# Kernel tuning notes

Measured on AMD Instinct MI355X. Metric: run time of the kernel, lower is better.

The kernel has to match this reference:

```python
import jax, jax.numpy as jnp
from jax import lax
import numpy as np

N = 8000                      # number of input points (also padded unique-voxel count)
PC_RANGE = (-50.0, -50.0, -3.0, 50.0, 50.0, 3.0)
VOXEL = (0.25, 0.25, 6.0)     # cluster_voxel_size
CONN_DIST = 0.6               # connected_dist
GX = int(np.floor((PC_RANGE[3] - PC_RANGE[0]) / VOXEL[0])) + 1
GY = int(np.floor((PC_RANGE[4] - PC_RANGE[1]) / VOXEL[1])) + 1
GZ = int(np.floor((PC_RANGE[5] - PC_RANGE[2]) / VOXEL[2])) + 1


def setup_inputs() -> dict:
    key = jax.random.key(0)
    u = jax.random.uniform(key, (N, 3), dtype=jnp.float32)
    lo = jnp.array(PC_RANGE[:3], jnp.float32)
    hi = jnp.array(PC_RANGE[3:], jnp.float32)
    points = lo + u * (hi - lo)          # points spread over the full pc_range
    batch_idx = jnp.zeros((N,), jnp.int32)  # single batch (eval path)
    return {"points": points, "batch_idx": batch_idx}


def _voxel_ids(points, batch_idx):
    lo = jnp.array(PC_RANGE[:3], dtype=points.dtype)
    vs = jnp.array(VOXEL, dtype=points.dtype)
    coors = jnp.floor((points - lo) / vs).astype(jnp.int32)
    coors = jnp.clip(coors, 0, jnp.array([GX - 1, GY - 1, GZ - 1], jnp.int32))
    # linearize (batch, cx, cy, cz) -> single int id (equivalent to unique over rows)
    return ((batch_idx * GX + coors[:, 0]) * GY + coors[:, 1]) * GZ + coors[:, 2]


def reference(points, batch_idx):
    # ---- scatter_v2(mode='avg'): voxelize + per-voxel mean ----
    vid = _voxel_ids(points, batch_idx)
    _, inv = jnp.unique(vid, size=N, fill_value=-1, return_inverse=True)
    inv = inv.reshape(-1)
    ones = jnp.ones((N,), points.dtype)
    counts = jax.ops.segment_sum(ones, inv, num_segments=N)           # [N]
    centers = jax.ops.segment_sum(points, inv, num_segments=N) / jnp.maximum(counts, 1.0)[:, None]
    valid = counts > 0                                                # real (non-padded) voxels

    # ---- radius adjacency over xy of voxel centers ----
    xy = centers[:, :2]
    sq = jnp.sum(xy * xy, axis=1)
    d2 = sq[:, None] + sq[None, :] - 2.0 * (xy @ xy.T)
    dmat = jnp.sqrt(jnp.maximum(d2, 0.0))                             # [N,N]
    pair_valid = valid[:, None] & valid[None, :]
    adj = (jnp.where(pair_valid, dmat, jnp.inf) < CONN_DIST) | jnp.eye(N, dtype=bool)

    # ---- connected components via min-label propagation + pointer jumping ----
    labels0 = jnp.arange(N, dtype=jnp.int32)

    def body_fn(state):
        l, _ = state
        nl = jnp.min(jnp.where(adj, l[None, :], N), axis=1).astype(jnp.int32)
        nl = jnp.minimum(nl, nl[nl])  # pointer jump accelerates convergence
        return (nl, jnp.all(nl == l))

    labels, _ = lax.while_loop(lambda st: jnp.logical_not(st[1]), body_fn, (labels0, jnp.array(False)))

    # compress component roots to dense 0..K-1 in first-occurrence order
    # (scipy.connected_components labels components by min node index order);
    # padded slots are pushed after all real components.
    comp_key = jnp.where(valid, labels, labels + N)
    _, comp = jnp.unique(comp_key, size=N, fill_value=2 * N, return_inverse=True)
    comp = comp.reshape(-1).astype(jnp.int32)

    cluster_inds = comp[inv]                                          # per-point component id
    cls = jnp.zeros((N,), jnp.int32)                                  # modify_cluster_by_class, class 0
    cluster_inds_per_point = jnp.stack([cls, batch_idx, cluster_inds], axis=1)  # [N,3]
    valid_mask = jnp.ones((N,), bool)                                 # min_points=1 -> all kept
    return cluster_inds_per_point, valid_mask
```

## Files before the change

kernel.cpp:

```cpp
#include <hip/hip_runtime.h>
#include <math.h>
#include <limits.h>

#define NPTS   8000
#define GXD    401
#define GYD    401
#define GZD    2
#define MVOX   321602
#define TS     256
#define NTB    32

__global__ void k_vid(const float* __restrict__ pts, const int* __restrict__ batch,
                      int* __restrict__ vid, int* __restrict__ V) {
  int p = blockIdx.x * blockDim.x + threadIdx.x;
  if (p >= NPTS) return;
  float x = pts[3 * p + 0], y = pts[3 * p + 1], z = pts[3 * p + 2];
  int cx = (int)floorf((x - (-50.0f)) / 0.25f);
  int cy = (int)floorf((y - (-50.0f)) / 0.25f);
  int cz = (int)floorf((z - (-3.0f)) / 6.0f);
  cx = min(max(cx, 0), GXD - 1);
  cy = min(max(cy, 0), GYD - 1);
  cz = min(max(cz, 0), GZD - 1);
  int b = batch[p];
  int v = ((b * GXD + cx) * GYD + cy) * GZD + cz;
  v = min(max(v, 0), MVOX - 1);
  vid[p] = v;
  atomicMin(&V[v], p);
}

__global__ void k_rank(const int* __restrict__ vid, const int* __restrict__ V,
                       int* __restrict__ inv) {
  __shared__ int rs[TS];
  int t = threadIdx.x;
  int j = blockIdx.y * TS + t;
  int r = INT_MAX;
  if (j < NPTS) {
    int v = vid[j];
    r = (V[v] == j) ? v : INT_MAX;
  }
  rs[t] = r;
  __syncthreads();
  int p = blockIdx.x * blockDim.x + t;
  if (p >= NPTS) return;
  int v = vid[p];
  int c = 0;
  const int4* rs4 = (const int4*)rs;
  #pragma unroll 16
  for (int k4 = 0; k4 < TS / 4; ++k4) {
    int4 q = rs4[k4];
    c += (q.x < v) ? 1 : 0;
    c += (q.y < v) ? 1 : 0;
    c += (q.z < v) ? 1 : 0;
    c += (q.w < v) ? 1 : 0;
  }
  if (c) atomicAdd(&inv[p], c);
}

__global__ void k_accum(const float* __restrict__ pts, const int* __restrict__ inv,
                        float* __restrict__ cnt, float* __restrict__ sx,
                        float* __restrict__ sy, int* __restrict__ parent) {
  int p = blockIdx.x * blockDim.x + threadIdx.x;
  if (p >= NPTS) return;
  parent[p] = p;
  int s = inv[p];
  atomicAdd(&cnt[s], 1.0f);
  atomicAdd(&sx[s], pts[3 * p + 0]);
  atomicAdd(&sy[s], pts[3 * p + 1]);
}

__global__ void k_centers(const float* __restrict__ cnt, const float* __restrict__ sx,
                          const float* __restrict__ sy, float4* __restrict__ pk) {
  int u = blockIdx.x * blockDim.x + threadIdx.x;
  if (u >= NPTS) return;
  float c = cnt[u];
  float d = fmaxf(c, 1.0f);
  float X = sx[u] / d;
  float Y = sy[u] / d;
  if (c > 0.0f) pk[u] = make_float4(X, Y, X * X + Y * Y, 0.0f);
  else          pk[u] = make_float4(0.0f, 0.0f, 1e30f, 0.0f);
}

__device__ __forceinline__ int load_par(int* parent, int x) {
  return __hip_atomic_load(&parent[x], __ATOMIC_RELAXED, __HIP_MEMORY_SCOPE_AGENT);
}

__device__ void hook(int* parent, int u, int v) {
  int ru = u, rv = v;
  while (true) {
    int p;
    while ((p = load_par(parent, ru)) != ru) ru = p;
    while ((p = load_par(parent, rv)) != rv) rv = p;
    if (ru == rv) return;
    int hi = ru > rv ? ru : rv;
    int lo = ru ^ rv ^ hi;
    int old = atomicCAS(&parent[hi], hi, lo);
    if (old == hi) return;
    ru = lo; rv = old;
  }
}

__global__ void k_edges(const float4* __restrict__ pk, int* __restrict__ parent) {
  if (blockIdx.y < blockIdx.x) return;
  __shared__ float4 tile[TS];
  int t = threadIdx.x;
  int j0 = blockIdx.y * TS;
  int j = j0 + t;
  tile[t] = (j < NPTS) ? pk[j] : make_float4(0.0f, 0.0f, 1e30f, 0.0f);
  __syncthreads();
  int i = blockIdx.x * blockDim.x + t;
  if (i >= NPTS) return;
  float4 qi = pk[i];
  float xi = qi.x, yi = qi.y, si = qi.z;
  for (int kb = 0; kb < TS; kb += 64) {
    unsigned long long m = 0;
    #pragma unroll
    for (int k2 = 0; k2 < 64; ++k2) {
      float4 q = tile[kb + k2];
      float d2 = si + q.z - 2.0f * (xi * q.x + yi * q.y);
      if (d2 < 0.36f) m |= (1ull << k2);
    }
    while (m) {
      int k2 = __ffsll(m) - 1;
      m &= m - 1;
      hook(parent, i, j0 + kb + k2);
    }
  }
}

__global__ void k_flatten(const int* __restrict__ parent, int* __restrict__ labels) {
  int u = blockIdx.x * blockDim.x + threadIdx.x;
  if (u >= NPTS) return;
  int x = u, p;
  while ((p = parent[x]) != x) x = p;
  labels[u] = x;
}

__global__ void k_scan(const int* __restrict__ labels, const float* __restrict__ cnt,
                       int* __restrict__ compRank) {
  __shared__ int sc[1024];
  int t = threadIdx.x;
  int f[8];
  int s = 0;
  #pragma unroll
  for (int k = 0; k < 8; ++k) {
    int i = t * 8 + k;
    int fl = 0;
    if (i < NPTS) fl = (cnt[i] > 0.0f && labels[i] == i) ? 1 : 0;
    f[k] = fl; s += fl;
  }
  sc[t] = s;
  __syncthreads();
  for (int off = 1; off < 1024; off <<= 1) {
    int v = sc[t];
    int a = (t >= off) ? sc[t - off] : 0;
    __syncthreads();
    sc[t] = v + a;
    __syncthreads();
  }
  int excl = sc[t] - s;
  #pragma unroll
  for (int k = 0; k < 8; ++k) {
    int i = t * 8 + k;
    if (i < NPTS) { compRank[i] = excl; excl += f[k]; }
  }
}

__global__ void k_out(const int* __restrict__ inv, const int* __restrict__ labels,
                      const int* __restrict__ compRank, const int* __restrict__ batch,
                      int* __restrict__ out) {
  int p = blockIdx.x * blockDim.x + threadIdx.x;
  if (p >= NPTS) return;
  int lab = labels[inv[p]];
  int c = compRank[lab];
  out[3 * p + 0] = 0;
  out[3 * p + 1] = batch[p];
  out[3 * p + 2] = c;
  out[3 * NPTS + p] = 1;
}

extern "C" void kernel_launch(void* const* d_in, const int* in_sizes, int n_in,
                              void* d_out, int out_size, void* d_ws, size_t ws_size,
                              hipStream_t stream) {
  const float* pts   = (const float*)d_in[0];
  const int*   batch = (const int*)d_in[1];
  int* out = (int*)d_out;

  char* base = (char*)d_ws;
  size_t o = 0;
  int*    V       = (int*)(base + o);    o += ((size_t)MVOX * 4 + 255) & ~(size_t)255;
  int*    vid     = (int*)(base + o);    o += NPTS * 4;
  int*    inv     = (int*)(base + o);    o += NPTS * 4;
  float*  cnt     = (float*)(base + o);  o += NPTS * 4;
  float*  sx      = (float*)(base + o);  o += NPTS * 4;
  float*  sy      = (float*)(base + o);  o += NPTS * 4;
  float4* pk      = (float4*)(base + o); o += (size_t)NPTS * 16;
  int*    parent  = (int*)(base + o);    o += NPTS * 4;
  int*    labels  = (int*)(base + o);    o += NPTS * 4;
  int*    compRank= (int*)(base + o);    o += NPTS * 4;

  hipMemsetAsync(V, 0x7F, (size_t)MVOX * 4, stream);
  hipMemsetAsync(inv, 0, (size_t)4 * NPTS * 4, stream);

  dim3 b256(256);
  dim3 g1((NPTS + 255) / 256);
  dim3 g2(NTB, NTB);

  k_vid<<<g1, b256, 0, stream>>>(pts, batch, vid, V);
  k_rank<<<g2, b256, 0, stream>>>(vid, V, inv);
  k_accum<<<g1, b256, 0, stream>>>(pts, inv, cnt, sx, sy, parent);
  k_centers<<<g1, b256, 0, stream>>>(cnt, sx, sy, pk);
  k_edges<<<g2, b256, 0, stream>>>(pk, parent);
  k_flatten<<<g1, b256, 0, stream>>>(parent, labels);
  k_scan<<<1, 1024, 0, stream>>>(labels, cnt, compRank);
  k_out<<<g1, b256, 0, stream>>>(inv, labels, compRank, batch, out);
}
```

Before: 112.7 us.

## Fuse all voxelize and clustering stages into one cooperative persistent kernel

Replaces the two memsets and eight separate kernel launches with a single cooperative kernel of 256 blocks that runs each stage in turn, separated by grid-wide syncs. Workspace initialization moves into the kernel, and the rank and edge tile loops become grid-stride loops over block pairs. Flatten and scan run concurrently in one phase: block 0 scans root flags while the other blocks flatten labels. This removes per-launch overhead and memset calls, in exchange for grid.sync costs and a fixed occupancy requirement for a cooperative launch.

```diff
diff --git a/kernel.cpp b/kernel.cpp
--- a/kernel.cpp
+++ b/kernel.cpp
@@ -1,6 +1,9 @@
 #include <hip/hip_runtime.h>
+#include <hip/hip_cooperative_groups.h>
 #include <math.h>
 #include <limits.h>
+
+namespace cg = cooperative_groups;
 
 #define NPTS   8000
 #define GXD    401
@@ -9,76 +12,10 @@
 #define MVOX   321602
 #define TS     256
 #define NTB    32
-
-__global__ void k_vid(const float* __restrict__ pts, const int* __restrict__ batch,
-                      int* __restrict__ vid, int* __restrict__ V) {
-  int p = blockIdx.x * blockDim.x + threadIdx.x;
-  if (p >= NPTS) return;
-  float x = pts[3 * p + 0], y = pts[3 * p + 1], z = pts[3 * p + 2];
-  int cx = (int)floorf((x - (-50.0f)) / 0.25f);
-  int cy = (int)floorf((y - (-50.0f)) / 0.25f);
-  int cz = (int)floorf((z - (-3.0f)) / 6.0f);
-  cx = min(max(cx, 0), GXD - 1);
-  cy = min(max(cy, 0), GYD - 1);
-  cz = min(max(cz, 0), GZD - 1);
-  int b = batch[p];
-  int v = ((b * GXD + cx) * GYD + cy) * GZD + cz;
-  v = min(max(v, 0), MVOX - 1);
-  vid[p] = v;
-  atomicMin(&V[v], p);
-}
-
-__global__ void k_rank(const int* __restrict__ vid, const int* __restrict__ V,
-                       int* __restrict__ inv) {
-  __shared__ int rs[TS];
-  int t = threadIdx.x;
-  int j = blockIdx.y * TS + t;
-  int r = INT_MAX;
-  if (j < NPTS) {
-    int v = vid[j];
-    r = (V[v] == j) ? v : INT_MAX;
-  }
-  rs[t] = r;
-  __syncthreads();
-  int p = blockIdx.x * blockDim.x + t;
-  if (p >= NPTS) return;
-  int v = vid[p];
-  int c = 0;
-  const int4* rs4 = (const int4*)rs;
-  #pragma unroll 16
-  for (int k4 = 0; k4 < TS / 4; ++k4) {
-    int4 q = rs4[k4];
-    c += (q.x < v) ? 1 : 0;
-    c += (q.y < v) ? 1 : 0;
-    c += (q.z < v) ? 1 : 0;
-    c += (q.w < v) ? 1 : 0;
-  }
-  if (c) atomicAdd(&inv[p], c);
-}
-
-__global__ void k_accum(const float* __restrict__ pts, const int* __restrict__ inv,
-                        float* __restrict__ cnt, float* __restrict__ sx,
-                        float* __restrict__ sy, int* __restrict__ parent) {
-  int p = blockIdx.x * blockDim.x + threadIdx.x;
-  if (p >= NPTS) return;
-  parent[p] = p;
-  int s = inv[p];
-  atomicAdd(&cnt[s], 1.0f);
-  atomicAdd(&sx[s], pts[3 * p + 0]);
-  atomicAdd(&sy[s], pts[3 * p + 1]);
-}
-
-__global__ void k_centers(const float* __restrict__ cnt, const float* __restrict__ sx,
-                          const float* __restrict__ sy, float4* __restrict__ pk) {
-  int u = blockIdx.x * blockDim.x + threadIdx.x;
-  if (u >= NPTS) return;
-  float c = cnt[u];
-  float d = fmaxf(c, 1.0f);
-  float X = sx[u] / d;
-  float Y = sy[u] / d;
-  if (c > 0.0f) pk[u] = make_float4(X, Y, X * X + Y * Y, 0.0f);
-  else          pk[u] = make_float4(0.0f, 0.0f, 1e30f, 0.0f);
-}
+#define NPAIR  528
+#define NBLK   256
+#define NTHR   256
+#define GSZ    (NBLK * NTHR)
 
 __device__ __forceinline__ int load_par(int* parent, int x) {
   return __hip_atomic_load(&parent[x], __ATOMIC_RELAXED, __HIP_MEMORY_SCOPE_AGENT);
@@ -99,83 +36,165 @@
   }
 }
 
-__global__ void k_edges(const float4* __restrict__ pk, int* __restrict__ parent) {
-  if (blockIdx.y < blockIdx.x) return;
+__global__ __launch_bounds__(NTHR, 2) void k_fused(
+    const float* __restrict__ pts, const int* __restrict__ batch,
+    int* V, int* vid, int* inv, float* cnt, float* sx, float* sy,
+    float4* pk, int* parent, int* labels, int* compRank, int* __restrict__ out)
+{
+  cg::grid_group grid = cg::this_grid();
+  const int t = threadIdx.x;
+  const int b = blockIdx.x;
+  const int g = b * NTHR + t;
+
+  __shared__ alignas(16) int rs[TS];
   __shared__ float4 tile[TS];
-  int t = threadIdx.x;
-  int j0 = blockIdx.y * TS;
-  int j = j0 + t;
-  tile[t] = (j < NPTS) ? pk[j] : make_float4(0.0f, 0.0f, 1e30f, 0.0f);
-  __syncthreads();
-  int i = blockIdx.x * blockDim.x + t;
-  if (i >= NPTS) return;
-  float4 qi = pk[i];
-  float xi = qi.x, yi = qi.y, si = qi.z;
-  for (int kb = 0; kb < TS; kb += 64) {
-    unsigned long long m = 0;
+  __shared__ int sc[NTHR];
+
+  for (int v = g; v < MVOX; v += GSZ) V[v] = INT_MAX;
+  if (g < NPTS) { inv[g] = 0; cnt[g] = 0.0f; sx[g] = 0.0f; sy[g] = 0.0f; }
+  grid.sync();
+
+  if (g < NPTS) {
+    float x = pts[3 * g + 0], y = pts[3 * g + 1], z = pts[3 * g + 2];
+    int cx = (int)floorf((x + 50.0f) / 0.25f);
+    int cy = (int)floorf((y + 50.0f) / 0.25f);
+    int cz = (int)floorf((z + 3.0f) / 6.0f);
+    cx = min(max(cx, 0), GXD - 1);
+    cy = min(max(cy, 0), GYD - 1);
+    cz = min(max(cz, 0), GZD - 1);
+    int bb = batch[g];
+    int v = ((bb * GXD + cx) * GYD + cy) * GZD + cz;
+    v = min(max(v, 0), MVOX - 1);
+    vid[g] = v;
+    atomicMin(&V[v], g);
+  }
+  grid.sync();
+
+  for (int vp = b; vp < NTB * NTB; vp += NBLK) {
+    int bx = vp & (NTB - 1);
+    int by = vp >> 5;
+    int j = by * TS + t;
+    int r = INT_MAX;
+    if (j < NPTS) {
+      int vv = vid[j];
+      r = (V[vv] == j) ? vv : INT_MAX;
+    }
+    __syncthreads();
+    rs[t] = r;
+    __syncthreads();
+    int p = bx * TS + t;
+    if (p < NPTS) {
+      int v = vid[p];
+      int c = 0;
+      const int4* rs4 = (const int4*)rs;
+      #pragma unroll 16
+      for (int k4 = 0; k4 < TS / 4; ++k4) {
+        int4 q = rs4[k4];
+        c += (q.x < v) ? 1 : 0;
+        c += (q.y < v) ? 1 : 0;
+        c += (q.z < v) ? 1 : 0;
+        c += (q.w < v) ? 1 : 0;
+      }
+      if (c) atomicAdd(&inv[p], c);
+    }
+  }
+  grid.sync();
+
+  if (g < NPTS) {
+    parent[g] = g;
+    int s = inv[g];
+    atomicAdd(&cnt[s], 1.0f);
+    atomicAdd(&sx[s], pts[3 * g + 0]);
+    atomicAdd(&sy[s], pts[3 * g + 1]);
+  }
+  grid.sync();
+
+  if (g < NPTS) {
+    float c = cnt[g];
+    float d = fmaxf(c, 1.0f);
+    float X = sx[g] / d;
+    float Y = sy[g] / d;
+    pk[g] = (c > 0.0f) ? make_float4(X, Y, X * X + Y * Y, 0.0f)
+                       : make_float4(0.0f, 0.0f, 1e30f, 0.0f);
+  }
+  grid.sync();
+
+  for (int e = b; e < NPAIR; e += NBLK) {
+    int by = (int)((sqrtf(8.0f * (float)e + 1.0f) - 1.0f) * 0.5f);
+    while ((by + 1) * (by + 2) / 2 <= e) ++by;
+    while (by * (by + 1) / 2 > e) --by;
+    int bx = e - by * (by + 1) / 2;
+    int j0 = by * TS;
+    int j = j0 + t;
+    __syncthreads();
+    tile[t] = (j < NPTS) ? pk[j] : make_float4(0.0f, 0.0f, 1e30f, 0.0f);
+    __syncthreads();
+    int i = bx * TS + t;
+    if (i < NPTS) {
+      float4 qi = pk[i];
+      float xi = qi.x, yi = qi.y, si = qi.z;
+      for (int kb = 0; kb < TS; kb += 64) {
+        unsigned long long m = 0;
+        #pragma unroll
+        for (int k2 = 0; k2 < 64; ++k2) {
+          float4 q = tile[kb + k2];
+          float d2 = si + q.z - 2.0f * (xi * q.x + yi * q.y);
+          if (d2 < 0.36f) m |= (1ull << k2);
+        }
+        while (m) {
+          int k2 = __ffsll(m) - 1;
+          m &= m - 1;
+          hook(parent, i, j0 + kb + k2);
+        }
+      }
+    }
+  }
+  grid.sync();
+
+  if (b == 0) {
+    unsigned flags = 0;
+    int base = t * 32;
+    int s = 0;
     #pragma unroll
-    for (int k2 = 0; k2 < 64; ++k2) {
-      float4 q = tile[kb + k2];
-      float d2 = si + q.z - 2.0f * (xi * q.x + yi * q.y);
-      if (d2 < 0.36f) m |= (1ull << k2);
-    }
-    while (m) {
-      int k2 = __ffsll(m) - 1;
-      m &= m - 1;
-      hook(parent, i, j0 + kb + k2);
-    }
-  }
-}
-
-__global__ void k_flatten(const int* __restrict__ parent, int* __restrict__ labels) {
-  int u = blockIdx.x * blockDim.x + threadIdx.x;
-  if (u >= NPTS) return;
-  int x = u, p;
-  while ((p = parent[x]) != x) x = p;
-  labels[u] = x;
-}
-
-__global__ void k_scan(const int* __restrict__ labels, const float* __restrict__ cnt,
-                       int* __restrict__ compRank) {
-  __shared__ int sc[1024];
-  int t = threadIdx.x;
-  int f[8];
-  int s = 0;
-  #pragma unroll
-  for (int k = 0; k < 8; ++k) {
-    int i = t * 8 + k;
-    int fl = 0;
-    if (i < NPTS) fl = (cnt[i] > 0.0f && labels[i] == i) ? 1 : 0;
-    f[k] = fl; s += fl;
-  }
-  sc[t] = s;
-  __syncthreads();
-  for (int off = 1; off < 1024; off <<= 1) {
-    int v = sc[t];
-    int a = (t >= off) ? sc[t - off] : 0;
-    __syncthreads();
-    sc[t] = v + a;
-    __syncthreads();
-  }
-  int excl = sc[t] - s;
-  #pragma unroll
-  for (int k = 0; k < 8; ++k) {
-    int i = t * 8 + k;
-    if (i < NPTS) { compRank[i] = excl; excl += f[k]; }
-  }
-}
-
-__global__ void k_out(const int* __restrict__ inv, const int* __restrict__ labels,
-                      const int* __restrict__ compRank, const int* __restrict__ batch,
-                      int* __restrict__ out) {
-  int p = blockIdx.x * blockDim.x + threadIdx.x;
-  if (p >= NPTS) return;
-  int lab = labels[inv[p]];
-  int c = compRank[lab];
-  out[3 * p + 0] = 0;
-  out[3 * p + 1] = batch[p];
-  out[3 * p + 2] = c;
-  out[3 * NPTS + p] = 1;
+    for (int k = 0; k < 32; ++k) {
+      int i = base + k;
+      int fl = 0;
+      if (i < NPTS) fl = (cnt[i] > 0.0f && load_par(parent, i) == i) ? 1 : 0;
+      flags |= (unsigned)fl << k;
+      s += fl;
+    }
+    sc[t] = s;
+    __syncthreads();
+    for (int off = 1; off < NTHR; off <<= 1) {
+      int v = sc[t];
+      int a = (t >= off) ? sc[t - off] : 0;
+      __syncthreads();
+      sc[t] = v + a;
+      __syncthreads();
+    }
+    int excl = sc[t] - s;
+    #pragma unroll
+    for (int k = 0; k < 32; ++k) {
+      int i = base + k;
+      if (i < NPTS) { compRank[i] = excl; excl += (flags >> k) & 1; }
+    }
+  } else {
+    int u = (b - 1) * NTHR + t;
+    if (u < NPTS) {
+      int x = u, p;
+      while ((p = parent[x]) != x) x = p;
+      labels[u] = x;
+    }
+  }
+  grid.sync();
+
+  if (g < NPTS) {
+    int lab = labels[inv[g]];
+    out[3 * g + 0] = 0;
+    out[3 * g + 1] = batch[g];
+    out[3 * g + 2] = compRank[lab];
+    out[3 * NPTS + g] = 1;
+  }
 }
 
 extern "C" void kernel_launch(void* const* d_in, const int* in_sizes, int n_in,
@@ -183,7 +202,7 @@
                               hipStream_t stream) {
   const float* pts   = (const float*)d_in[0];
   const int*   batch = (const int*)d_in[1];
-  int* out = (int*)d_out;
+  int* outp = (int*)d_out;
 
   char* base = (char*)d_ws;
   size_t o = 0;
@@ -198,19 +217,10 @@
   int*    labels  = (int*)(base + o);    o += NPTS * 4;
   int*    compRank= (int*)(base + o);    o += NPTS * 4;
 
-  hipMemsetAsync(V, 0x7F, (size_t)MVOX * 4, stream);
-  hipMemsetAsync(inv, 0, (size_t)4 * NPTS * 4, stream);
-
-  dim3 b256(256);
-  dim3 g1((NPTS + 255) / 256);
-  dim3 g2(NTB, NTB);
-
-  k_vid<<<g1, b256, 0, stream>>>(pts, batch, vid, V);
-  k_rank<<<g2, b256, 0, stream>>>(vid, V, inv);
-  k_accum<<<g1, b256, 0, stream>>>(pts, inv, cnt, sx, sy, parent);
-  k_centers<<<g1, b256, 0, stream>>>(cnt, sx, sy, pk);
-  k_edges<<<g2, b256, 0, stream>>>(pk, parent);
-  k_flatten<<<g1, b256, 0, stream>>>(parent, labels);
-  k_scan<<<1, 1024, 0, stream>>>(labels, cnt, compRank);
-  k_out<<<g1, b256, 0, stream>>>(inv, labels, compRank, batch, out);
-}
+  void* args[] = { (void*)&pts, (void*)&batch, (void*)&V, (void*)&vid,
+                   (void*)&inv, (void*)&cnt, (void*)&sx, (void*)&sy,
+                   (void*)&pk, (void*)&parent, (void*)&labels,
+                   (void*)&compRank, (void*)&outp };
+  hipLaunchCooperativeKernel((const void*)k_fused, dim3(NBLK), dim3(NTHR),
+                             args, 0, stream);
+}
```

Measured after the change: 295.9 us. +162.6%, slower.

## Fuse init, centers, flatten and scan kernels; launch only upper-triangle edge tiles

Applied to the files above, without the earlier changes.

Replaces the second memset by zeroing the accumulators inside k_vid and computes voxel centers on the fly inside k_edges, which removes k_centers and the packed buffer. The edge kernel now launches only the 528 upper-triangle tile pairs instead of a 32x32 grid with early exit. Flatten and scan are merged into one launch where block 0 scans using a parent[i]==i root test and the other blocks flatten labels. This cuts launch overhead and idle blocks, at the cost of recomputing centers per tile and a triangular index decode.

```diff
diff --git a/kernel.cpp b/kernel.cpp
--- a/kernel.cpp
+++ b/kernel.cpp
@@ -9,15 +9,19 @@
 #define MVOX   321602
 #define TS     256
 #define NTB    32
+#define NPAIR  528
 
 __global__ void k_vid(const float* __restrict__ pts, const int* __restrict__ batch,
-                      int* __restrict__ vid, int* __restrict__ V) {
+                      int* __restrict__ vid, int* __restrict__ V,
+                      int* __restrict__ inv, float* __restrict__ cnt,
+                      float* __restrict__ sx, float* __restrict__ sy) {
   int p = blockIdx.x * blockDim.x + threadIdx.x;
   if (p >= NPTS) return;
+  inv[p] = 0; cnt[p] = 0.0f; sx[p] = 0.0f; sy[p] = 0.0f;
   float x = pts[3 * p + 0], y = pts[3 * p + 1], z = pts[3 * p + 2];
-  int cx = (int)floorf((x - (-50.0f)) / 0.25f);
-  int cy = (int)floorf((y - (-50.0f)) / 0.25f);
-  int cz = (int)floorf((z - (-3.0f)) / 6.0f);
+  int cx = (int)floorf((x + 50.0f) / 0.25f);
+  int cy = (int)floorf((y + 50.0f) / 0.25f);
+  int cz = (int)floorf((z + 3.0f) / 6.0f);
   cx = min(max(cx, 0), GXD - 1);
   cy = min(max(cy, 0), GYD - 1);
   cz = min(max(cz, 0), GZD - 1);
@@ -30,17 +34,17 @@
 
 __global__ void k_rank(const int* __restrict__ vid, const int* __restrict__ V,
                        int* __restrict__ inv) {
-  __shared__ int rs[TS];
+  __shared__ alignas(16) int rs[TS];
   int t = threadIdx.x;
   int j = blockIdx.y * TS + t;
   int r = INT_MAX;
   if (j < NPTS) {
-    int v = vid[j];
-    r = (V[v] == j) ? v : INT_MAX;
+    int vv = vid[j];
+    r = (V[vv] == j) ? vv : INT_MAX;
   }
   rs[t] = r;
   __syncthreads();
-  int p = blockIdx.x * blockDim.x + t;
+  int p = blockIdx.x * TS + t;
   if (p >= NPTS) return;
   int v = vid[p];
   int c = 0;
@@ -66,18 +70,6 @@
   atomicAdd(&cnt[s], 1.0f);
   atomicAdd(&sx[s], pts[3 * p + 0]);
   atomicAdd(&sy[s], pts[3 * p + 1]);
-}
-
-__global__ void k_centers(const float* __restrict__ cnt, const float* __restrict__ sx,
-                          const float* __restrict__ sy, float4* __restrict__ pk) {
-  int u = blockIdx.x * blockDim.x + threadIdx.x;
-  if (u >= NPTS) return;
-  float c = cnt[u];
-  float d = fmaxf(c, 1.0f);
-  float X = sx[u] / d;
-  float Y = sy[u] / d;
-  if (c > 0.0f) pk[u] = make_float4(X, Y, X * X + Y * Y, 0.0f);
-  else          pk[u] = make_float4(0.0f, 0.0f, 1e30f, 0.0f);
 }
 
 __device__ __forceinline__ int load_par(int* parent, int x) {
@@ -99,17 +91,33 @@
   }
 }
 
-__global__ void k_edges(const float4* __restrict__ pk, int* __restrict__ parent) {
-  if (blockIdx.y < blockIdx.x) return;
+__device__ __forceinline__ float4 center_of(int u, const float* cnt,
+                                            const float* sx, const float* sy) {
+  float c = cnt[u];
+  float d = fmaxf(c, 1.0f);
+  float X = sx[u] / d;
+  float Y = sy[u] / d;
+  float sq = (c > 0.0f) ? (X * X + Y * Y) : 1e30f;
+  return make_float4(X, Y, sq, 0.0f);
+}
+
+__global__ void k_edges(const float* __restrict__ cnt, const float* __restrict__ sx,
+                        const float* __restrict__ sy, int* __restrict__ parent) {
   __shared__ float4 tile[TS];
   int t = threadIdx.x;
-  int j0 = blockIdx.y * TS;
+  int e = blockIdx.x;
+  int by = (int)((sqrtf(8.0f * (float)e + 1.0f) - 1.0f) * 0.5f);
+  while ((by + 1) * (by + 2) / 2 <= e) ++by;
+  while (by * (by + 1) / 2 > e) --by;
+  int bx = e - by * (by + 1) / 2;
+  int j0 = by * TS;
   int j = j0 + t;
-  tile[t] = (j < NPTS) ? pk[j] : make_float4(0.0f, 0.0f, 1e30f, 0.0f);
+  tile[t] = (j < NPTS) ? center_of(j, cnt, sx, sy)
+                       : make_float4(0.0f, 0.0f, 1e30f, 0.0f);
   __syncthreads();
-  int i = blockIdx.x * blockDim.x + t;
+  int i = bx * TS + t;
   if (i >= NPTS) return;
-  float4 qi = pk[i];
+  float4 qi = center_of(i, cnt, sx, sy);
   float xi = qi.x, yi = qi.y, si = qi.z;
   for (int kb = 0; kb < TS; kb += 64) {
     unsigned long long m = 0;
@@ -127,41 +135,45 @@
   }
 }
 
-__global__ void k_flatten(const int* __restrict__ parent, int* __restrict__ labels) {
-  int u = blockIdx.x * blockDim.x + threadIdx.x;
-  if (u >= NPTS) return;
-  int x = u, p;
-  while ((p = parent[x]) != x) x = p;
-  labels[u] = x;
-}
-
-__global__ void k_scan(const int* __restrict__ labels, const float* __restrict__ cnt,
-                       int* __restrict__ compRank) {
-  __shared__ int sc[1024];
+__global__ void k_post(int* __restrict__ parent, const float* __restrict__ cnt,
+                       int* __restrict__ labels, int* __restrict__ compRank) {
   int t = threadIdx.x;
-  int f[8];
-  int s = 0;
-  #pragma unroll
-  for (int k = 0; k < 8; ++k) {
-    int i = t * 8 + k;
-    int fl = 0;
-    if (i < NPTS) fl = (cnt[i] > 0.0f && labels[i] == i) ? 1 : 0;
-    f[k] = fl; s += fl;
-  }
-  sc[t] = s;
-  __syncthreads();
-  for (int off = 1; off < 1024; off <<= 1) {
-    int v = sc[t];
-    int a = (t >= off) ? sc[t - off] : 0;
+  int b = blockIdx.x;
+  if (b == 0) {
+    __shared__ int sc[TS];
+    unsigned flags = 0;
+    int base = t * 32;
+    int s = 0;
+    #pragma unroll
+    for (int k = 0; k < 32; ++k) {
+      int i = base + k;
+      int fl = 0;
+      if (i < NPTS) fl = (cnt[i] > 0.0f && parent[i] == i) ? 1 : 0;
+      flags |= (unsigned)fl << k;
+      s += fl;
+    }
+    sc[t] = s;
     __syncthreads();
-    sc[t] = v + a;
-    __syncthreads();
-  }
-  int excl = sc[t] - s;
-  #pragma unroll
-  for (int k = 0; k < 8; ++k) {
-    int i = t * 8 + k;
-    if (i < NPTS) { compRank[i] = excl; excl += f[k]; }
+    for (int off = 1; off < TS; off <<= 1) {
+      int v = sc[t];
+      int a = (t >= off) ? sc[t - off] : 0;
+      __syncthreads();
+      sc[t] = v + a;
+      __syncthreads();
+    }
+    int excl = sc[t] - s;
+    #pragma unroll
+    for (int k = 0; k < 32; ++k) {
+      int i = base + k;
+      if (i < NPTS) { compRank[i] = excl; excl += (flags >> k) & 1; }
+    }
+  } else {
+    int u = (b - 1) * TS + t;
+    if (u < NPTS) {
+      int x = u, p;
+      while ((p = parent[x]) != x) x = p;
+      labels[u] = x;
+    }
   }
 }
 
@@ -171,10 +183,9 @@
   int p = blockIdx.x * blockDim.x + threadIdx.x;
   if (p >= NPTS) return;
   int lab = labels[inv[p]];
-  int c = compRank[lab];
   out[3 * p + 0] = 0;
   out[3 * p + 1] = batch[p];
-  out[3 * p + 2] = c;
+  out[3 * p + 2] = compRank[lab];
   out[3 * NPTS + p] = 1;
 }
 
@@ -183,34 +194,27 @@
                               hipStream_t stream) {
   const float* pts   = (const float*)d_in[0];
   const int*   batch = (const int*)d_in[1];
-  int* out = (int*)d_out;
+  int* outp = (int*)d_out;
 
   char* base = (char*)d_ws;
   size_t o = 0;
-  int*    V       = (int*)(base + o);    o += ((size_t)MVOX * 4 + 255) & ~(size_t)255;
-  int*    vid     = (int*)(base + o);    o += NPTS * 4;
-  int*    inv     = (int*)(base + o);    o += NPTS * 4;
-  float*  cnt     = (float*)(base + o);  o += NPTS * 4;
-  float*  sx      = (float*)(base + o);  o += NPTS * 4;
-  float*  sy      = (float*)(base + o);  o += NPTS * 4;
-  float4* pk      = (float4*)(base + o); o += (size_t)NPTS * 16;
-  int*    parent  = (int*)(base + o);    o += NPTS * 4;
-  int*    labels  = (int*)(base + o);    o += NPTS * 4;
-  int*    compRank= (int*)(base + o);    o += NPTS * 4;
+  int*   V       = (int*)(base + o);   o += ((size_t)MVOX * 4 + 255) & ~(size_t)255;
+  int*   vid     = (int*)(base + o);   o += NPTS * 4;
+  int*   inv     = (int*)(base + o);   o += NPTS * 4;
+  float* cnt     = (float*)(base + o); o += NPTS * 4;
+  float* sx      = (float*)(base + o); o += NPTS * 4;
+  float* sy      = (float*)(base + o); o += NPTS * 4;
+  int*   parent  = (int*)(base + o);   o += NPTS * 4;
+  int*   labels  = (int*)(base + o);   o += NPTS * 4;
+  int*   compRank= (int*)(base + o);   o += NPTS * 4;
 
   hipMemsetAsync(V, 0x7F, (size_t)MVOX * 4, stream);
-  hipMemsetAsync(inv, 0, (size_t)4 * NPTS * 4, stream);
-
-  dim3 b256(256);
-  dim3 g1((NPTS + 255) / 256);
-  dim3 g2(NTB, NTB);
-
-  k_vid<<<g1, b256, 0, stream>>>(pts, batch, vid, V);
-  k_rank<<<g2, b256, 0, stream>>>(vid, V, inv);
-  k_accum<<<g1, b256, 0, stream>>>(pts, inv, cnt, sx, sy, parent);
-  k_centers<<<g1, b256, 0, stream>>>(cnt, sx, sy, pk);
-  k_edges<<<g2, b256, 0, stream>>>(pk, parent);
-  k_flatten<<<g1, b256, 0, stream>>>(parent, labels);
-  k_scan<<<1, 1024, 0, stream>>>(labels, cnt, compRank);
-  k_out<<<g1, b256, 0, stream>>>(inv, labels, compRank, batch, out);
-}
+
+  dim3 b256(TS);
+  k_vid  <<<dim3(NTB),       b256, 0, stream>>>(pts, batch, vid, V, inv, cnt, sx, sy);
+  k_rank <<<dim3(NTB, NTB),  b256, 0, stream>>>(vid, V, inv);
+  k_accum<<<dim3(NTB),       b256, 0, stream>>>(pts, inv, cnt, sx, sy, parent);
+  k_edges<<<dim3(NPAIR),     b256, 0, stream>>>(cnt, sx, sy, parent);
+  k_post <<<dim3(NTB + 1),   b256, 0, stream>>>(parent, cnt, labels, compRank);
+  k_out  <<<dim3(NTB),       b256, 0, stream>>>(inv, labels, compRank, batch, outp);
+}
```

Measured after the change: 105.9 us. -6.0%, faster.
